# Performance work log

Measured on AMD Instinct MI355X. Metric: run time of the kernel, lower is better.

Reference implementation:

```python
import jax, jax.numpy as jnp
import numpy as np

N_NODES = 50000
N_EDGES = 800000
F_DIM = 256
H_DIM = 256
O_DIM = 64


def spmm(edge_index, edge_weight, x):
    # sparse adj (COO) @ dense x: out[dst] += w * x[src]
    src = edge_index[0]
    dst = edge_index[1]
    msgs = edge_weight[:, None] * x[src]          # [E, D]
    return jax.ops.segment_sum(msgs, dst, num_segments=x.shape[0])


def setup_inputs() -> dict:
    key = jax.random.key(0)
    ks = jax.random.split(key, 10)
    stdv = 1.0 / np.sqrt(H_DIM)
    u = lambda k, shp: jax.random.uniform(k, shp, jnp.float32, -stdv, stdv)
    return {
        "input": jax.random.normal(ks[0], (N_NODES, F_DIM), jnp.float32),
        "edge_index": jax.random.randint(ks[1], (2, N_EDGES), 0, N_NODES, jnp.int32),
        "edge_weight": jax.random.uniform(ks[2], (N_EDGES,), jnp.float32),
        "mixture_weight": u(ks[3], (1,)),
        "hidden_weight": u(ks[4], (F_DIM, H_DIM)),
        "hidden_bias": u(ks[5], (H_DIM,)),
        "mean_weight": u(ks[6], (H_DIM, O_DIM)),
        "mean_bias": u(ks[7], (O_DIM,)),
        "log_std_weight": u(ks[8], (H_DIM, O_DIM)),
        "log_std_bias": u(ks[9], (O_DIM,)),
    }


def reference(input, edge_index, edge_weight, mixture_weight, hidden_weight,
              hidden_bias, mean_weight, mean_bias, log_std_weight, log_std_bias):
    # eval mode: dropout is identity
    # --- GCN branch ---
    support = input @ hidden_weight                       # [N, H]
    hidden_g = jax.nn.relu(spmm(edge_index, edge_weight, support) + hidden_bias)
    mean_gcn = spmm(edge_index, edge_weight, hidden_g @ mean_weight)      # [N, O]
    log_std_gcn = spmm(edge_index, edge_weight, hidden_g @ log_std_weight)
    # --- MLP branch ---
    hidden_m = jax.nn.relu(support + hidden_bias)
    mean_mlp = hidden_m @ mean_weight + mean_bias
    log_std_mlp = hidden_m @ log_std_weight + log_std_bias
    # --- mixture (note: z_mean uses raw weight, z_log_std uses sigmoid, as in source) ---
    mw = mixture_weight
    mr = jax.nn.sigmoid(mixture_weight)
    z_mean = mean_gcn * mw + mean_mlp * (1.0 - mw)
    z_log_std = log_std_gcn * mr + log_std_mlp * (1.0 - mr)
    return (z_mean, z_log_std)
```

## Files before the change

kernel.cpp:

```cpp
#include <hip/hip_runtime.h>
#include <math.h>

#define NN 50000
#define NE 800000
#define KD 256
#define OD 64
#define NCH ((NN + 255) / 256)
#define EPB 4096
#define NBLK ((NE + EPB - 1) / EPB)
#define NHT (NCH * NBLK)

#define QS 32.0f
#define IQS (1.0f / 32.0f)
#define QS2 16.0f
#define IQS2 (1.0f / 16.0f)

using bf16x8 = __attribute__((ext_vector_type(8))) short;
using f32x4  = __attribute__((ext_vector_type(4))) float;

__device__ __forceinline__ unsigned short f2b(float x) {
    union { float f; unsigned u; } c; c.f = x;
    unsigned r = (c.u + 0x7FFF + ((c.u >> 16) & 1)) >> 16;
    return (unsigned short)r;
}
__device__ __forceinline__ float b2f(unsigned short b) {
    union { unsigned u; float f; } c; c.u = ((unsigned)b) << 16;
    return c.f;
}
__device__ __forceinline__ signed char quant8(float v) {
    int q = __float2int_rn(v * QS);
    q = q > 127 ? 127 : (q < -127 ? -127 : q);
    return (signed char)q;
}
__device__ __forceinline__ unsigned quant16u(float v) {
    int q = __float2int_rn(v * QS2);
    return (unsigned)(q > 127 ? 127 : q);
}

__device__ __forceinline__ void blk_scan(int* s, int t) {
    for (int o = 1; o < 256; o <<= 1) {
        int x = (t >= o) ? s[t - o] : 0;
        __syncthreads();
        s[t] += x;
        __syncthreads();
    }
}


__global__ __launch_bounds__(256) void k_histconv(const int* __restrict__ dst,
                                                  int* __restrict__ histT,
                                                  const float* __restrict__ hw,
                                                  const float* __restrict__ mw_,
                                                  const float* __restrict__ lw,
                                                  unsigned short* __restrict__ Wht,
                                                  unsigned short* __restrict__ Wmlt) {
    __shared__ int bins[NCH];
    int t = threadIdx.x;
    if (blockIdx.x < NBLK) {
        int blk = blockIdx.x;
        if (t < NCH) bins[t] = 0;
        __syncthreads();
        int base = blk * EPB;
        #pragma unroll
        for (int i = 0; i < EPB / 256; ++i) {
            int e = base + i * 256 + t;
            if (e < NE) atomicAdd(&bins[dst[e] >> 8], 1);
        }
        __syncthreads();
        if (t < NCH) histT[t * NBLK + blk] = bins[t];
    } else {
        int idx = (blockIdx.x - NBLK) * 256 + t;
        if (idx < 256 * 256) {
            int n = idx >> 8, k = idx & 255;
            Wht[(size_t)n * 256 + k] = f2b(hw[(size_t)k * 256 + n]);
        }
        if (idx < 128 * 256) {
            int n = idx >> 8, k = idx & 255;
            float v = (n < 64) ? mw_[(size_t)k * 64 + n] : lw[(size_t)k * 64 + (n - 64)];
            Wmlt[(size_t)n * 256 + k] = f2b(v);
        }
    }
}

__global__ __launch_bounds__(256) void k_scanbins(int* __restrict__ histT,
                                                  int* __restrict__ binSum) {
    __shared__ int s[256];
    int bin = blockIdx.x, t = threadIdx.x;
    int v = (t < NBLK) ? histT[bin * NBLK + t] : 0;
    s[t] = v;
    __syncthreads();
    blk_scan(s, t);
    if (t < NBLK) histT[bin * NBLK + t] = s[t] - v;
    if (t == NBLK - 1) binSum[bin] = s[t];
}

__global__ __launch_bounds__(256) void k_bucketw(const int* __restrict__ src,
                                                 const int* __restrict__ dst,
                                                 const float* __restrict__ w,
                                                 const int* __restrict__ histT,
                                                 const int* __restrict__ binSum,
                                                 int2* __restrict__ bkt) {
    __shared__ int pre[256];
    __shared__ int cur[NCH];
    int t = threadIdx.x, blk = blockIdx.x;
    int v = (t < NCH) ? binSum[t] : 0;
    pre[t] = v;
    __syncthreads();
    blk_scan(pre, t);
    if (t < NCH) cur[t] = histT[t * NBLK + blk] + (pre[t] - v);
    __syncthreads();
    int base = blk * EPB;
    #pragma unroll
    for (int i = 0; i < EPB / 256; ++i) {
        int e = base + i * 256 + t;
        if (e < NE) {
            int d = dst[e];
            int p = atomicAdd(&cur[d >> 8], 1);
            bkt[p] = make_int2((d << 16) | src[e], __float_as_int(w[e]));
        }
    }
}

__global__ __launch_bounds__(256) void k_deg2(const int2* __restrict__ bkt,
                                              const int* __restrict__ binSum,
                                              int* __restrict__ deg,
                                              int* __restrict__ chunkSum8) {
    __shared__ int incl[256];
    __shared__ int cnt[256];
    int t = threadIdx.x, b = blockIdx.x;
    incl[t] = (t < NCH) ? binSum[t] : 0;
    cnt[t] = 0;
    __syncthreads();
    blk_scan(incl, t);
    int e0 = (b > 0) ? incl[b - 1] : 0;
    int e1 = incl[b];
    __syncthreads();
    for (int e = e0 + t; e < e1; e += 256)
        atomicAdd(&cnt[(((unsigned)bkt[e].x) >> 16) & 255], 1);
    __syncthreads();
    int node = b * 256 + t;
    int c = cnt[t];
    if (node < NN) deg[node] = c;
    __shared__ int s[256];
    s[t] = (node < NN) ? ((c + 7) & ~7) : 0;
    __syncthreads();
    for (int o = 128; o > 0; o >>= 1) {
        if (t < o) s[t] += s[t + o];
        __syncthreads();
    }
    if (t == 0) chunkSum8[b] = s[0];
}

__global__ __launch_bounds__(256) void k_place2f(const int2* __restrict__ bkt,
                                                 const int* __restrict__ binSum,
                                                 const int* __restrict__ chunkSum8,
                                                 const int* __restrict__ deg,
                                                 int* __restrict__ offsets8,
                                                 int2* __restrict__ pedge) {
    __shared__ int binc[256];
    __shared__ int cinc[256];
    __shared__ int s[256];
    __shared__ int ncur[256];
    int t = threadIdx.x, b = blockIdx.x;
    binc[t] = (t < NCH) ? binSum[t] : 0;
    __syncthreads();
    blk_scan(binc, t);
    cinc[t] = (t < NCH) ? chunkSum8[t] : 0;
    __syncthreads();
    blk_scan(cinc, t);
    int e0 = (b > 0) ? binc[b - 1] : 0;
    int e1 = binc[b];
    int chunkBase = (b > 0) ? cinc[b - 1] : 0;
    __syncthreads();
    int node = b * 256 + t;
    int dv = (node < NN) ? deg[node] : 0;
    int pv = (dv + 7) & ~7;
    s[t] = pv;
    __syncthreads();
    blk_scan(s, t);
    int excl = s[t] - pv + chunkBase;
    if (node <= NN) offsets8[node] = excl;
    ncur[t] = excl;
    __syncthreads();
    for (int e = e0 + t; e < e1; e += 256) {
        int2 v = bkt[e];
        int d = ((unsigned)v.x) >> 16;
        int p = atomicAdd(&ncur[d & 255], 1);
        pedge[p] = v;
    }
    __syncthreads();
    if (node < NN) {
        int p0 = ncur[t];
        int p1 = excl + pv;
        for (int p = p0; p < p1; ++p) pedge[p] = make_int2(0, 0);
    }
}


__global__ __launch_bounds__(256) void k_gemm1(const float* __restrict__ Ap,
                                               const unsigned short* __restrict__ Bt,
                                               signed char* __restrict__ supqOut) {
    __shared__ unsigned short As[64 * 64];
    __shared__ unsigned short Bs[128 * 64];
    const int tid = threadIdx.x;
    const int row0 = (blockIdx.x >> 1) * 64;
    const int n0 = (blockIdx.x & 1) * 128;
    const int lane = tid & 63;
    const int w = tid >> 6, wm = w >> 1, wn = w & 1;
    const int lr = lane & 15, lg = lane >> 4;
    const int rA = tid >> 2, qA = tid & 3;
    const int rB = tid >> 1, hB = tid & 1;

    f32x4 acc[2][4] = {};

    for (int k0 = 0; k0 < KD; k0 += 64) {
        {
            int gr = row0 + rA;
            unsigned short tmp[16];
            if (gr < NN) {
                #pragma unroll
                for (int i = 0; i < 4; ++i) {
                    float4 v = *reinterpret_cast<const float4*>(
                        &Ap[(size_t)gr * KD + k0 + qA * 16 + i * 4]);
                    tmp[i * 4 + 0] = f2b(v.x); tmp[i * 4 + 1] = f2b(v.y);
                    tmp[i * 4 + 2] = f2b(v.z); tmp[i * 4 + 3] = f2b(v.w);
                }
            } else {
                #pragma unroll
                for (int i = 0; i < 16; ++i) tmp[i] = 0;
            }
            int s0 = (qA * 2) ^ (rA & 7);
            int s1 = (qA * 2 + 1) ^ (rA & 7);
            *reinterpret_cast<uint4*>(&As[rA * 64 + s0 * 8]) = *reinterpret_cast<const uint4*>(&tmp[0]);
            *reinterpret_cast<uint4*>(&As[rA * 64 + s1 * 8]) = *reinterpret_cast<const uint4*>(&tmp[8]);
        }
        {
            const unsigned short* B = Bt + (size_t)(n0 + rB) * KD + k0 + hB * 32;
            #pragma unroll
            for (int i = 0; i < 4; ++i) {
                uint4 u = *reinterpret_cast<const uint4*>(B + i * 8);
                int slot = (hB * 4 + i) ^ (rB & 7);
                *reinterpret_cast<uint4*>(&Bs[rB * 64 + slot * 8]) = u;
            }
        }
        __syncthreads();
        #pragma unroll
        for (int ks = 0; ks < 2; ++ks) {
            int slot = ks * 4 + lg;
            bf16x8 a[2], b[4];
            #pragma unroll
            for (int fm = 0; fm < 2; ++fm) {
                int ra = wm * 32 + fm * 16 + lr;
                a[fm] = *reinterpret_cast<const bf16x8*>(&As[ra * 64 + ((slot ^ (ra & 7))) * 8]);
            }
            #pragma unroll
            for (int fn = 0; fn < 4; ++fn) {
                int rb = wn * 64 + fn * 16 + lr;
                b[fn] = *reinterpret_cast<const bf16x8*>(&Bs[rb * 64 + ((slot ^ (rb & 7))) * 8]);
            }
            #pragma unroll
            for (int fm = 0; fm < 2; ++fm)
                #pragma unroll
                for (int fn = 0; fn < 4; ++fn)
                    acc[fm][fn] = __builtin_amdgcn_mfma_f32_16x16x32_bf16(a[fm], b[fn], acc[fm][fn], 0, 0, 0);
        }
        __syncthreads();
    }
    #pragma unroll
    for (int fm = 0; fm < 2; ++fm) {
        #pragma unroll
        for (int j = 0; j < 4; ++j) {
            int grow = row0 + wm * 32 + fm * 16 + lg * 4 + j;
            if (grow >= NN) continue;
            #pragma unroll
            for (int fn = 0; fn < 4; ++fn) {
                int gcol = n0 + wn * 64 + fn * 16 + lr;
                supqOut[(size_t)grow * 256 + gcol] = quant8(acc[fm][fn][j]);
            }
        }
    }
}


__global__ __launch_bounds__(256) void k_gemm2(const signed char* __restrict__ hgq,
                                               const signed char* __restrict__ supq,
                                               const unsigned short* __restrict__ Bt,
                                               const float* __restrict__ hbias,
                                               const float* __restrict__ mbias,
                                               const float* __restrict__ lbias,
                                               signed char* __restrict__ gcnq,
                                               unsigned short* __restrict__ mlpout) {
    __shared__ unsigned short As[64 * 64];
    __shared__ unsigned short Bs[128 * 64];
    const bool mlpMode = blockIdx.y != 0;
    const int tid = threadIdx.x;
    const int row0 = blockIdx.x * 64;
    const int lane = tid & 63;
    const int w = tid >> 6, wm = w >> 1, wn = w & 1;
    const int lr = lane & 15, lg = lane >> 4;
    const int rA = tid >> 2, qA = tid & 3;
    const int rB = tid >> 1, hB = tid & 1;

    f32x4 acc[2][4] = {};

    for (int k0 = 0; k0 < KD; k0 += 64) {
        {
            int gr = row0 + rA;
            unsigned short tmp[16];
            if (gr < NN) {
                signed char q[16];
                const signed char* Aq = mlpMode ? supq : hgq;
                *reinterpret_cast<uint4*>(q) =
                    *reinterpret_cast<const uint4*>(&Aq[(size_t)gr * KD + k0 + qA * 16]);
                if (mlpMode) {
                    #pragma unroll
                    for (int i = 0; i < 4; ++i) {
                        float4 hb4 = *reinterpret_cast<const float4*>(&hbias[k0 + qA * 16 + i * 4]);
                        tmp[i * 4 + 0] = f2b(fmaxf((float)q[i * 4 + 0] * IQS + hb4.x, 0.f));
                        tmp[i * 4 + 1] = f2b(fmaxf((float)q[i * 4 + 1] * IQS + hb4.y, 0.f));
                        tmp[i * 4 + 2] = f2b(fmaxf((float)q[i * 4 + 2] * IQS + hb4.z, 0.f));
                        tmp[i * 4 + 3] = f2b(fmaxf((float)q[i * 4 + 3] * IQS + hb4.w, 0.f));
                    }
                } else {
                    #pragma unroll
                    for (int i = 0; i < 16; ++i) tmp[i] = f2b((float)q[i] * IQS2);
                }
            } else {
                #pragma unroll
                for (int i = 0; i < 16; ++i) tmp[i] = 0;
            }
            int s0 = (qA * 2) ^ (rA & 7);
            int s1 = (qA * 2 + 1) ^ (rA & 7);
            *reinterpret_cast<uint4*>(&As[rA * 64 + s0 * 8]) = *reinterpret_cast<const uint4*>(&tmp[0]);
            *reinterpret_cast<uint4*>(&As[rA * 64 + s1 * 8]) = *reinterpret_cast<const uint4*>(&tmp[8]);
        }
        {
            const unsigned short* B = Bt + (size_t)rB * KD + k0 + hB * 32;
            #pragma unroll
            for (int i = 0; i < 4; ++i) {
                uint4 u = *reinterpret_cast<const uint4*>(B + i * 8);
                int slot = (hB * 4 + i) ^ (rB & 7);
                *reinterpret_cast<uint4*>(&Bs[rB * 64 + slot * 8]) = u;
            }
        }
        __syncthreads();
        #pragma unroll
        for (int ks = 0; ks < 2; ++ks) {
            int slot = ks * 4 + lg;
            bf16x8 a[2], b[4];
            #pragma unroll
            for (int fm = 0; fm < 2; ++fm) {
                int ra = wm * 32 + fm * 16 + lr;
                a[fm] = *reinterpret_cast<const bf16x8*>(&As[ra * 64 + ((slot ^ (ra & 7))) * 8]);
            }
            #pragma unroll
            for (int fn = 0; fn < 4; ++fn) {
                int rb = wn * 64 + fn * 16 + lr;
                b[fn] = *reinterpret_cast<const bf16x8*>(&Bs[rb * 64 + ((slot ^ (rb & 7))) * 8]);
            }
            #pragma unroll
            for (int fm = 0; fm < 2; ++fm)
                #pragma unroll
                for (int fn = 0; fn < 4; ++fn)
                    acc[fm][fn] = __builtin_amdgcn_mfma_f32_16x16x32_bf16(a[fm], b[fn], acc[fm][fn], 0, 0, 0);
        }
        __syncthreads();
    }
    #pragma unroll
    for (int fm = 0; fm < 2; ++fm) {
        #pragma unroll
        for (int j = 0; j < 4; ++j) {
            int grow = row0 + wm * 32 + fm * 16 + lg * 4 + j;
            if (grow >= NN) continue;
            #pragma unroll
            for (int fn = 0; fn < 4; ++fn) {
                int gcol = wn * 64 + fn * 16 + lr;
                float v = acc[fm][fn][j];
                if (mlpMode) {
                    float b = (gcol < 64) ? mbias[gcol] : lbias[gcol - 64];
                    mlpout[(size_t)grow * 128 + gcol] = f2b(v + b);
                } else {
                    gcnq[(size_t)grow * 128 + gcol] = quant8(v);
                }
            }
        }
    }
}


__global__ __launch_bounds__(256) void k_spmm1(const int* __restrict__ off8,
                                               const int2* __restrict__ pedge,
                                               const unsigned* __restrict__ supq,
                                               const float* __restrict__ bias,
                                               unsigned* __restrict__ hgq) {
    int lane = threadIdx.x & 63;
    int wid = blockIdx.x * 4 + (threadIdx.x >> 6);
    int d0 = wid * 2, d1 = d0 + 1;
    int ea = off8[d0], eA = off8[d0 + 1], eB = off8[d0 + 2];
    int eb = eA;
    float a0 = 0.f, a1 = 0.f, a2 = 0.f, a3 = 0.f;
    float c0 = 0.f, c1 = 0.f, c2 = 0.f, c3 = 0.f;
    for (; ea < eA && eb < eB; ea += 8, eb += 8) {
        int2 Ea[8], Eb[8];
        unsigned Ua[8], Ub[8];
        #pragma unroll
        for (int i = 0; i < 8; ++i) { Ea[i] = pedge[ea + i]; Eb[i] = pedge[eb + i]; }
        #pragma unroll
        for (int i = 0; i < 8; ++i) {
            Ua[i] = supq[(size_t)(Ea[i].x & 0xffff) * 64 + lane];
            Ub[i] = supq[(size_t)(Eb[i].x & 0xffff) * 64 + lane];
        }
        #pragma unroll
        for (int i = 0; i < 8; ++i) {
            float wa = __int_as_float(Ea[i].y), wb = __int_as_float(Eb[i].y);
            unsigned ua = Ua[i], ub = Ub[i];
            a0 = fmaf(wa, (float)((int)(signed char)(ua)), a0);
            a1 = fmaf(wa, (float)((int)(signed char)(ua >> 8)), a1);
            a2 = fmaf(wa, (float)((int)(signed char)(ua >> 16)), a2);
            a3 = fmaf(wa, (float)((int)(signed char)(ua >> 24)), a3);
            c0 = fmaf(wb, (float)((int)(signed char)(ub)), c0);
            c1 = fmaf(wb, (float)((int)(signed char)(ub >> 8)), c1);
            c2 = fmaf(wb, (float)((int)(signed char)(ub >> 16)), c2);
            c3 = fmaf(wb, (float)((int)(signed char)(ub >> 24)), c3);
        }
    }
    for (; ea < eA; ea += 8) {
        int2 E[8]; unsigned U[8];
        #pragma unroll
        for (int i = 0; i < 8; ++i) E[i] = pedge[ea + i];
        #pragma unroll
        for (int i = 0; i < 8; ++i) U[i] = supq[(size_t)(E[i].x & 0xffff) * 64 + lane];
        #pragma unroll
        for (int i = 0; i < 8; ++i) {
            float w = __int_as_float(E[i].y); unsigned u = U[i];
            a0 = fmaf(w, (float)((int)(signed char)(u)), a0);
            a1 = fmaf(w, (float)((int)(signed char)(u >> 8)), a1);
            a2 = fmaf(w, (float)((int)(signed char)(u >> 16)), a2);
            a3 = fmaf(w, (float)((int)(signed char)(u >> 24)), a3);
        }
    }
    for (; eb < eB; eb += 8) {
        int2 E[8]; unsigned U[8];
        #pragma unroll
        for (int i = 0; i < 8; ++i) E[i] = pedge[eb + i];
        #pragma unroll
        for (int i = 0; i < 8; ++i) U[i] = supq[(size_t)(E[i].x & 0xffff) * 64 + lane];
        #pragma unroll
        for (int i = 0; i < 8; ++i) {
            float w = __int_as_float(E[i].y); unsigned u = U[i];
            c0 = fmaf(w, (float)((int)(signed char)(u)), c0);
            c1 = fmaf(w, (float)((int)(signed char)(u >> 8)), c1);
            c2 = fmaf(w, (float)((int)(signed char)(u >> 16)), c2);
            c3 = fmaf(w, (float)((int)(signed char)(u >> 24)), c3);
        }
    }
    float4 b = *reinterpret_cast<const float4*>(&bias[lane * 4]);
    unsigned oa = quant16u(fmaxf(a0 * IQS + b.x, 0.f))
                | (quant16u(fmaxf(a1 * IQS + b.y, 0.f)) << 8)
                | (quant16u(fmaxf(a2 * IQS + b.z, 0.f)) << 16)
                | (quant16u(fmaxf(a3 * IQS + b.w, 0.f)) << 24);
    unsigned oc = quant16u(fmaxf(c0 * IQS + b.x, 0.f))
                | (quant16u(fmaxf(c1 * IQS + b.y, 0.f)) << 8)
                | (quant16u(fmaxf(c2 * IQS + b.z, 0.f)) << 16)
                | (quant16u(fmaxf(c3 * IQS + b.w, 0.f)) << 24);
    hgq[(size_t)d0 * 64 + lane] = oa;
    hgq[(size_t)d1 * 64 + lane] = oc;
}


__global__ __launch_bounds__(256) void k_spmm2(const int* __restrict__ off8,
                                               const int2* __restrict__ pedge,
                                               const unsigned short* __restrict__ gq,
                                               const unsigned short* __restrict__ mlp,
                                               const float* __restrict__ mixw,
                                               float* __restrict__ out) {
    int lane = threadIdx.x & 63;
    int wid = blockIdx.x * 4 + (threadIdx.x >> 6);
    int d0 = wid * 2, d1 = d0 + 1;
    int ea = off8[d0], eA = off8[d0 + 1], eB = off8[d0 + 2];
    int eb = eA;
    float a0 = 0.f, a1 = 0.f, c0 = 0.f, c1 = 0.f;
    for (; ea < eA && eb < eB; ea += 8, eb += 8) {
        int2 Ea[8], Eb[8];
        unsigned short Ua[8], Ub[8];
        #pragma unroll
        for (int i = 0; i < 8; ++i) { Ea[i] = pedge[ea + i]; Eb[i] = pedge[eb + i]; }
        #pragma unroll
        for (int i = 0; i < 8; ++i) {
            Ua[i] = gq[(size_t)(Ea[i].x & 0xffff) * 64 + lane];
            Ub[i] = gq[(size_t)(Eb[i].x & 0xffff) * 64 + lane];
        }
        #pragma unroll
        for (int i = 0; i < 8; ++i) {
            float wa = __int_as_float(Ea[i].y), wb = __int_as_float(Eb[i].y);
            a0 = fmaf(wa, (float)((int)(signed char)(Ua[i] & 0xff)), a0);
            a1 = fmaf(wa, (float)((int)(signed char)(Ua[i] >> 8)), a1);
            c0 = fmaf(wb, (float)((int)(signed char)(Ub[i] & 0xff)), c0);
            c1 = fmaf(wb, (float)((int)(signed char)(Ub[i] >> 8)), c1);
        }
    }
    for (; ea < eA; ea += 8) {
        int2 E[8]; unsigned short U[8];
        #pragma unroll
        for (int i = 0; i < 8; ++i) E[i] = pedge[ea + i];
        #pragma unroll
        for (int i = 0; i < 8; ++i) U[i] = gq[(size_t)(E[i].x & 0xffff) * 64 + lane];
        #pragma unroll
        for (int i = 0; i < 8; ++i) {
            float w = __int_as_float(E[i].y);
            a0 = fmaf(w, (float)((int)(signed char)(U[i] & 0xff)), a0);
            a1 = fmaf(w, (float)((int)(signed char)(U[i] >> 8)), a1);
        }
    }
    for (; eb < eB; eb += 8) {
        int2 E[8]; unsigned short U[8];
        #pragma unroll
        for (int i = 0; i < 8; ++i) E[i] = pedge[eb + i];
        #pragma unroll
        for (int i = 0; i < 8; ++i) U[i] = gq[(size_t)(E[i].x & 0xffff) * 64 + lane];
        #pragma unroll
        for (int i = 0; i < 8; ++i) {
            float w = __int_as_float(E[i].y);
            c0 = fmaf(w, (float)((int)(signed char)(U[i] & 0xff)), c0);
            c1 = fmaf(w, (float)((int)(signed char)(U[i] >> 8)), c1);
        }
    }
    float mw = mixw[0];
    float mr = 1.f / (1.f + expf(-mw));
    int c = lane * 2;
    ushort2 mu0 = reinterpret_cast<const ushort2*>(mlp)[(size_t)d0 * 64 + lane];
    ushort2 mu1 = reinterpret_cast<const ushort2*>(mlp)[(size_t)d1 * 64 + lane];
    float g00 = a0 * IQS, g01 = a1 * IQS;
    float g10 = c0 * IQS, g11 = c1 * IQS;
    if (c < 64) {
        *reinterpret_cast<float2*>(out + (size_t)d0 * OD + c) =
            make_float2(g00 * mw + b2f(mu0.x) * (1.f - mw), g01 * mw + b2f(mu0.y) * (1.f - mw));
        *reinterpret_cast<float2*>(out + (size_t)d1 * OD + c) =
            make_float2(g10 * mw + b2f(mu1.x) * (1.f - mw), g11 * mw + b2f(mu1.y) * (1.f - mw));
    } else {
        float* ol = out + (size_t)NN * OD;
        *reinterpret_cast<float2*>(ol + (size_t)d0 * OD + (c - 64)) =
            make_float2(g00 * mr + b2f(mu0.x) * (1.f - mr), g01 * mr + b2f(mu0.y) * (1.f - mr));
        *reinterpret_cast<float2*>(ol + (size_t)d1 * OD + (c - 64)) =
            make_float2(g10 * mr + b2f(mu1.x) * (1.f - mr), g11 * mr + b2f(mu1.y) * (1.f - mr));
    }
}


extern "C" void kernel_launch(void* const* d_in, const int* in_sizes, int n_in,
                              void* d_out, int out_size, void* d_ws, size_t ws_size,
                              hipStream_t stream) {
    const float* input = (const float*)d_in[0];
    const int*   ei    = (const int*)d_in[1];
    const float* ew    = (const float*)d_in[2];
    const float* mixw  = (const float*)d_in[3];
    const float* hw    = (const float*)d_in[4];
    const float* hb    = (const float*)d_in[5];
    const float* mw_   = (const float*)d_in[6];
    const float* mb    = (const float*)d_in[7];
    const float* lw    = (const float*)d_in[8];
    const float* lb    = (const float*)d_in[9];
    float* out = (float*)d_out;

    const int* src = ei;
    const int* dst = ei + NE;

    char* ws = (char*)d_ws;
    size_t off = 0;
    auto alloc = [&](size_t bytes) -> void* {
        void* p = ws + off;
        off += (bytes + 255) & ~(size_t)255;
        return p;
    };
    int*   deg      = (int*)alloc((size_t)NN * 4);
    int*   offsets8 = (int*)alloc((size_t)(NN + 2) * 4);
    int*   chunkSum8= (int*)alloc((size_t)NCH * 4);
    int*   binSum   = (int*)alloc((size_t)NCH * 4);
    int*   histT    = (int*)alloc((size_t)NHT * 4);
    int2*  bkt      = (int2*)alloc((size_t)NE * 8);
    int2*  pedge    = (int2*)alloc(((size_t)NE + 8 * NN) * 8);
    unsigned short* Wht  = (unsigned short*)alloc((size_t)256 * 256 * 2);
    unsigned short* Wmlt = (unsigned short*)alloc((size_t)128 * 256 * 2);
    signed char*    supq     = (signed char*)alloc((size_t)NN * KD);
    signed char*    hgq      = (signed char*)alloc((size_t)NN * KD);
    signed char*    gcnq     = (signed char*)alloc((size_t)NN * 128);
    unsigned short* mlp      = (unsigned short*)alloc((size_t)NN * 128 * 2);

    k_histconv<<<NBLK + 256, 256, 0, stream>>>(dst, histT, hw, mw_, lw, Wht, Wmlt);
    k_scanbins<<<NCH, 256, 0, stream>>>(histT, binSum);
    k_bucketw<<<NBLK, 256, 0, stream>>>(src, dst, ew, histT, binSum, bkt);
    k_deg2<<<NCH, 256, 0, stream>>>(bkt, binSum, deg, chunkSum8);
    k_place2f<<<NCH, 256, 0, stream>>>(bkt, binSum, chunkSum8, deg, offsets8, pedge);

    int mblk = (NN + 63) / 64;
    k_gemm1<<<mblk * 2, 256, 0, stream>>>(input, Wht, supq);
    k_spmm1<<<NN / 8, 256, 0, stream>>>(offsets8, pedge, (const unsigned*)supq, hb, (unsigned*)hgq);
    k_gemm2<<<dim3(mblk, 2), 256, 0, stream>>>(hgq, supq, Wmlt, hb, mb, lb, gcnq, mlp);
    k_spmm2<<<NN / 8, 256, 0, stream>>>(offsets8, pedge, (const unsigned short*)gcnq, mlp, mixw, out);
}
```

Baseline: 150.9 us.

## Pack CSR edges into 32-bit bf16 weight plus index, four nodes per wave

Edge records in the padded CSR are packed into one 32-bit word holding a 16-bit source index and a bf16 weight, instead of an int2 with an fp32 weight. This halves the edge-stream traffic in both SpMM passes. Each wavefront now processes four destination nodes as two contiguous two-node segment streams, switching accumulators at the midpoint offset, and the SpMM grids shrink to match. The cost is reduced precision in the edge weights and extra branching per 8-edge chunk.

New measurement: 152.4 us. About the same (+1.0%).

```diff
diff --git a/kernel.cpp b/kernel.cpp
--- a/kernel.cpp
+++ b/kernel.cpp
@@ -156,7 +156,7 @@
                                                  const int* __restrict__ chunkSum8,
                                                  const int* __restrict__ deg,
                                                  int* __restrict__ offsets8,
-                                                 int2* __restrict__ pedge) {
+                                                 int* __restrict__ pedge) {
     __shared__ int binc[256];
     __shared__ int cinc[256];
     __shared__ int s[256];
@@ -186,13 +186,13 @@
         int2 v = bkt[e];
         int d = ((unsigned)v.x) >> 16;
         int p = atomicAdd(&ncur[d & 255], 1);
-        pedge[p] = v;
+        pedge[p] = (v.x & 0xffff) | ((int)f2b(__int_as_float(v.y)) << 16);
     }
     __syncthreads();
     if (node < NN) {
         int p0 = ncur[t];
         int p1 = excl + pv;
-        for (int p = p0; p < p1; ++p) pedge[p] = make_int2(0, 0);
+        for (int p = p0; p < p1; ++p) pedge[p] = 0;
     }
 }
 
@@ -389,160 +389,184 @@
 
 
 __global__ __launch_bounds__(256) void k_spmm1(const int* __restrict__ off8,
-                                               const int2* __restrict__ pedge,
+                                               const int* __restrict__ pedge,
                                                const unsigned* __restrict__ supq,
                                                const float* __restrict__ bias,
                                                unsigned* __restrict__ hgq) {
     int lane = threadIdx.x & 63;
     int wid = blockIdx.x * 4 + (threadIdx.x >> 6);
-    int d0 = wid * 2, d1 = d0 + 1;
-    int ea = off8[d0], eA = off8[d0 + 1], eB = off8[d0 + 2];
-    int eb = eA;
-    float a0 = 0.f, a1 = 0.f, a2 = 0.f, a3 = 0.f;
-    float c0 = 0.f, c1 = 0.f, c2 = 0.f, c3 = 0.f;
-    for (; ea < eA && eb < eB; ea += 8, eb += 8) {
-        int2 Ea[8], Eb[8];
+    int d0 = wid * 4;
+    int ea = off8[d0],     midA = off8[d0 + 1], eAend = off8[d0 + 2];
+    int eb = eAend,        midB = off8[d0 + 3], eBend = off8[d0 + 4];
+    float a0[4] = {}, a1[4] = {}, b0[4] = {}, b1[4] = {};
+
+    while (ea < eAend && eb < eBend) {
+        int Ea[8], Eb[8];
         unsigned Ua[8], Ub[8];
         #pragma unroll
         for (int i = 0; i < 8; ++i) { Ea[i] = pedge[ea + i]; Eb[i] = pedge[eb + i]; }
         #pragma unroll
         for (int i = 0; i < 8; ++i) {
-            Ua[i] = supq[(size_t)(Ea[i].x & 0xffff) * 64 + lane];
-            Ub[i] = supq[(size_t)(Eb[i].x & 0xffff) * 64 + lane];
-        }
-        #pragma unroll
-        for (int i = 0; i < 8; ++i) {
-            float wa = __int_as_float(Ea[i].y), wb = __int_as_float(Eb[i].y);
+            Ua[i] = supq[(size_t)(Ea[i] & 0xffff) * 64 + lane];
+            Ub[i] = supq[(size_t)(Eb[i] & 0xffff) * 64 + lane];
+        }
+        float tA[4] = {}, tB[4] = {};
+        #pragma unroll
+        for (int i = 0; i < 8; ++i) {
+            float wa = b2f((unsigned short)(((unsigned)Ea[i]) >> 16));
+            float wb = b2f((unsigned short)(((unsigned)Eb[i]) >> 16));
             unsigned ua = Ua[i], ub = Ub[i];
-            a0 = fmaf(wa, (float)((int)(signed char)(ua)), a0);
-            a1 = fmaf(wa, (float)((int)(signed char)(ua >> 8)), a1);
-            a2 = fmaf(wa, (float)((int)(signed char)(ua >> 16)), a2);
-            a3 = fmaf(wa, (float)((int)(signed char)(ua >> 24)), a3);
-            c0 = fmaf(wb, (float)((int)(signed char)(ub)), c0);
-            c1 = fmaf(wb, (float)((int)(signed char)(ub >> 8)), c1);
-            c2 = fmaf(wb, (float)((int)(signed char)(ub >> 16)), c2);
-            c3 = fmaf(wb, (float)((int)(signed char)(ub >> 24)), c3);
-        }
-    }
-    for (; ea < eA; ea += 8) {
-        int2 E[8]; unsigned U[8];
+            tA[0] = fmaf(wa, (float)((int)(signed char)(ua)), tA[0]);
+            tA[1] = fmaf(wa, (float)((int)(signed char)(ua >> 8)), tA[1]);
+            tA[2] = fmaf(wa, (float)((int)(signed char)(ua >> 16)), tA[2]);
+            tA[3] = fmaf(wa, (float)((int)(signed char)(ua >> 24)), tA[3]);
+            tB[0] = fmaf(wb, (float)((int)(signed char)(ub)), tB[0]);
+            tB[1] = fmaf(wb, (float)((int)(signed char)(ub >> 8)), tB[1]);
+            tB[2] = fmaf(wb, (float)((int)(signed char)(ub >> 16)), tB[2]);
+            tB[3] = fmaf(wb, (float)((int)(signed char)(ub >> 24)), tB[3]);
+        }
+        if (ea < midA) { a0[0]+=tA[0]; a0[1]+=tA[1]; a0[2]+=tA[2]; a0[3]+=tA[3]; }
+        else           { a1[0]+=tA[0]; a1[1]+=tA[1]; a1[2]+=tA[2]; a1[3]+=tA[3]; }
+        if (eb < midB) { b0[0]+=tB[0]; b0[1]+=tB[1]; b0[2]+=tB[2]; b0[3]+=tB[3]; }
+        else           { b1[0]+=tB[0]; b1[1]+=tB[1]; b1[2]+=tB[2]; b1[3]+=tB[3]; }
+        ea += 8; eb += 8;
+    }
+    for (; ea < eAend; ea += 8) {
+        int E[8]; unsigned U[8];
         #pragma unroll
         for (int i = 0; i < 8; ++i) E[i] = pedge[ea + i];
         #pragma unroll
-        for (int i = 0; i < 8; ++i) U[i] = supq[(size_t)(E[i].x & 0xffff) * 64 + lane];
-        #pragma unroll
-        for (int i = 0; i < 8; ++i) {
-            float w = __int_as_float(E[i].y); unsigned u = U[i];
-            a0 = fmaf(w, (float)((int)(signed char)(u)), a0);
-            a1 = fmaf(w, (float)((int)(signed char)(u >> 8)), a1);
-            a2 = fmaf(w, (float)((int)(signed char)(u >> 16)), a2);
-            a3 = fmaf(w, (float)((int)(signed char)(u >> 24)), a3);
-        }
-    }
-    for (; eb < eB; eb += 8) {
-        int2 E[8]; unsigned U[8];
+        for (int i = 0; i < 8; ++i) U[i] = supq[(size_t)(E[i] & 0xffff) * 64 + lane];
+        float tA[4] = {};
+        #pragma unroll
+        for (int i = 0; i < 8; ++i) {
+            float w = b2f((unsigned short)(((unsigned)E[i]) >> 16));
+            unsigned u = U[i];
+            tA[0] = fmaf(w, (float)((int)(signed char)(u)), tA[0]);
+            tA[1] = fmaf(w, (float)((int)(signed char)(u >> 8)), tA[1]);
+            tA[2] = fmaf(w, (float)((int)(signed char)(u >> 16)), tA[2]);
+            tA[3] = fmaf(w, (float)((int)(signed char)(u >> 24)), tA[3]);
+        }
+        if (ea < midA) { a0[0]+=tA[0]; a0[1]+=tA[1]; a0[2]+=tA[2]; a0[3]+=tA[3]; }
+        else           { a1[0]+=tA[0]; a1[1]+=tA[1]; a1[2]+=tA[2]; a1[3]+=tA[3]; }
+    }
+    for (; eb < eBend; eb += 8) {
+        int E[8]; unsigned U[8];
         #pragma unroll
         for (int i = 0; i < 8; ++i) E[i] = pedge[eb + i];
         #pragma unroll
-        for (int i = 0; i < 8; ++i) U[i] = supq[(size_t)(E[i].x & 0xffff) * 64 + lane];
-        #pragma unroll
-        for (int i = 0; i < 8; ++i) {
-            float w = __int_as_float(E[i].y); unsigned u = U[i];
-            c0 = fmaf(w, (float)((int)(signed char)(u)), c0);
-            c1 = fmaf(w, (float)((int)(signed char)(u >> 8)), c1);
-            c2 = fmaf(w, (float)((int)(signed char)(u >> 16)), c2);
-            c3 = fmaf(w, (float)((int)(signed char)(u >> 24)), c3);
-        }
-    }
-    float4 b = *reinterpret_cast<const float4*>(&bias[lane * 4]);
-    unsigned oa = quant16u(fmaxf(a0 * IQS + b.x, 0.f))
-                | (quant16u(fmaxf(a1 * IQS + b.y, 0.f)) << 8)
-                | (quant16u(fmaxf(a2 * IQS + b.z, 0.f)) << 16)
-                | (quant16u(fmaxf(a3 * IQS + b.w, 0.f)) << 24);
-    unsigned oc = quant16u(fmaxf(c0 * IQS + b.x, 0.f))
-                | (quant16u(fmaxf(c1 * IQS + b.y, 0.f)) << 8)
-                | (quant16u(fmaxf(c2 * IQS + b.z, 0.f)) << 16)
-                | (quant16u(fmaxf(c3 * IQS + b.w, 0.f)) << 24);
-    hgq[(size_t)d0 * 64 + lane] = oa;
-    hgq[(size_t)d1 * 64 + lane] = oc;
+        for (int i = 0; i < 8; ++i) U[i] = supq[(size_t)(E[i] & 0xffff) * 64 + lane];
+        float tB[4] = {};
+        #pragma unroll
+        for (int i = 0; i < 8; ++i) {
+            float w = b2f((unsigned short)(((unsigned)E[i]) >> 16));
+            unsigned u = U[i];
+            tB[0] = fmaf(w, (float)((int)(signed char)(u)), tB[0]);
+            tB[1] = fmaf(w, (float)((int)(signed char)(u >> 8)), tB[1]);
+            tB[2] = fmaf(w, (float)((int)(signed char)(u >> 16)), tB[2]);
+            tB[3] = fmaf(w, (float)((int)(signed char)(u >> 24)), tB[3]);
+        }
+        if (eb < midB) { b0[0]+=tB[0]; b0[1]+=tB[1]; b0[2]+=tB[2]; b0[3]+=tB[3]; }
+        else           { b1[0]+=tB[0]; b1[1]+=tB[1]; b1[2]+=tB[2]; b1[3]+=tB[3]; }
+    }
+    float4 bv = *reinterpret_cast<const float4*>(&bias[lane * 4]);
+    float* accs[4] = { a0, a1, b0, b1 };
+    #pragma unroll
+    for (int j = 0; j < 4; ++j) {
+        float* a = accs[j];
+        unsigned o = quant16u(fmaxf(a[0] * IQS + bv.x, 0.f))
+                   | (quant16u(fmaxf(a[1] * IQS + bv.y, 0.f)) << 8)
+                   | (quant16u(fmaxf(a[2] * IQS + bv.z, 0.f)) << 16)
+                   | (quant16u(fmaxf(a[3] * IQS + bv.w, 0.f)) << 24);
+        hgq[(size_t)(d0 + j) * 64 + lane] = o;
+    }
 }
 
 
 __global__ __launch_bounds__(256) void k_spmm2(const int* __restrict__ off8,
-                                               const int2* __restrict__ pedge,
+                                               const int* __restrict__ pedge,
                                                const unsigned short* __restrict__ gq,
                                                const unsigned short* __restrict__ mlp,
                                                const float* __restrict__ mixw,
                                                float* __restrict__ out) {
     int lane = threadIdx.x & 63;
     int wid = blockIdx.x * 4 + (threadIdx.x >> 6);
-    int d0 = wid * 2, d1 = d0 + 1;
-    int ea = off8[d0], eA = off8[d0 + 1], eB = off8[d0 + 2];
-    int eb = eA;
-    float a0 = 0.f, a1 = 0.f, c0 = 0.f, c1 = 0.f;
-    for (; ea < eA && eb < eB; ea += 8, eb += 8) {
-        int2 Ea[8], Eb[8];
+    int d0 = wid * 4;
+    int ea = off8[d0],     midA = off8[d0 + 1], eAend = off8[d0 + 2];
+    int eb = eAend,        midB = off8[d0 + 3], eBend = off8[d0 + 4];
+    float a0[2] = {}, a1[2] = {}, b0[2] = {}, b1[2] = {};
+
+    while (ea < eAend && eb < eBend) {
+        int Ea[8], Eb[8];
         unsigned short Ua[8], Ub[8];
         #pragma unroll
         for (int i = 0; i < 8; ++i) { Ea[i] = pedge[ea + i]; Eb[i] = pedge[eb + i]; }
         #pragma unroll
         for (int i = 0; i < 8; ++i) {
-            Ua[i] = gq[(size_t)(Ea[i].x & 0xffff) * 64 + lane];
-            Ub[i] = gq[(size_t)(Eb[i].x & 0xffff) * 64 + lane];
-        }
-        #pragma unroll
-        for (int i = 0; i < 8; ++i) {
-            float wa = __int_as_float(Ea[i].y), wb = __int_as_float(Eb[i].y);
-            a0 = fmaf(wa, (float)((int)(signed char)(Ua[i] & 0xff)), a0);
-            a1 = fmaf(wa, (float)((int)(signed char)(Ua[i] >> 8)), a1);
-            c0 = fmaf(wb, (float)((int)(signed char)(Ub[i] & 0xff)), c0);
-            c1 = fmaf(wb, (float)((int)(signed char)(Ub[i] >> 8)), c1);
-        }
-    }
-    for (; ea < eA; ea += 8) {
-        int2 E[8]; unsigned short U[8];
+            Ua[i] = gq[(size_t)(Ea[i] & 0xffff) * 64 + lane];
+            Ub[i] = gq[(size_t)(Eb[i] & 0xffff) * 64 + lane];
+        }
+        float tA[2] = {}, tB[2] = {};
+        #pragma unroll
+        for (int i = 0; i < 8; ++i) {
+            float wa = b2f((unsigned short)(((unsigned)Ea[i]) >> 16));
+            float wb = b2f((unsigned short)(((unsigned)Eb[i]) >> 16));
+            tA[0] = fmaf(wa, (float)((int)(signed char)(Ua[i] & 0xff)), tA[0]);
+            tA[1] = fmaf(wa, (float)((int)(signed char)(Ua[i] >> 8)), tA[1]);
+            tB[0] = fmaf(wb, (float)((int)(signed char)(Ub[i] & 0xff)), tB[0]);
+            tB[1] = fmaf(wb, (float)((int)(signed char)(Ub[i] >> 8)), tB[1]);
+        }
+        if (ea < midA) { a0[0]+=tA[0]; a0[1]+=tA[1]; } else { a1[0]+=tA[0]; a1[1]+=tA[1]; }
+        if (eb < midB) { b0[0]+=tB[0]; b0[1]+=tB[1]; } else { b1[0]+=tB[0]; b1[1]+=tB[1]; }
+        ea += 8; eb += 8;
+    }
+    for (; ea < eAend; ea += 8) {
+        int E[8]; unsigned short U[8];
         #pragma unroll
         for (int i = 0; i < 8; ++i) E[i] = pedge[ea + i];
         #pragma unroll
-        for (int i = 0; i < 8; ++i) U[i] = gq[(size_t)(E[i].x & 0xffff) * 64 + lane];
-        #pragma unroll
-        for (int i = 0; i < 8; ++i) {
-            float w = __int_as_float(E[i].y);
-            a0 = fmaf(w, (float)((int)(signed char)(U[i] & 0xff)), a0);
-            a1 = fmaf(w, (float)((int)(signed char)(U[i] >> 8)), a1);
-        }
-    }
-    for (; eb < eB; eb += 8) {
-        int2 E[8]; unsigned short U[8];
+        for (int i = 0; i < 8; ++i) U[i] = gq[(size_t)(E[i] & 0xffff) * 64 + lane];
+        float tA[2] = {};
+        #pragma unroll
+        for (int i = 0; i < 8; ++i) {
+            float w = b2f((unsigned short)(((unsigned)E[i]) >> 16));
+            tA[0] = fmaf(w, (float)((int)(signed char)(U[i] & 0xff)), tA[0]);
+            tA[1] = fmaf(w, (float)((int)(signed char)(U[i] >> 8)), tA[1]);
+        }
+        if (ea < midA) { a0[0]+=tA[0]; a0[1]+=tA[1]; } else { a1[0]+=tA[0]; a1[1]+=tA[1]; }
+    }
+    for (; eb < eBend; eb += 8) {
+        int E[8]; unsigned short U[8];
         #pragma unroll
         for (int i = 0; i < 8; ++i) E[i] = pedge[eb + i];
         #pragma unroll
-        for (int i = 0; i < 8; ++i) U[i] = gq[(size_t)(E[i].x & 0xffff) * 64 + lane];
-        #pragma unroll
-        for (int i = 0; i < 8; ++i) {
-            float w = __int_as_float(E[i].y);
-            c0 = fmaf(w, (float)((int)(signed char)(U[i] & 0xff)), c0);
-            c1 = fmaf(w, (float)((int)(signed char)(U[i] >> 8)), c1);
-        }
+        for (int i = 0; i < 8; ++i) U[i] = gq[(size_t)(E[i] & 0xffff) * 64 + lane];
+        float tB[2] = {};
+        #pragma unroll
+        for (int i = 0; i < 8; ++i) {
+            float w = b2f((unsigned short)(((unsigned)E[i]) >> 16));
+            tB[0] = fmaf(w, (float)((int)(signed char)(U[i] & 0xff)), tB[0]);
+            tB[1] = fmaf(w, (float)((int)(signed char)(U[i] >> 8)), tB[1]);
+        }
+        if (eb < midB) { b0[0]+=tB[0]; b0[1]+=tB[1]; } else { b1[0]+=tB[0]; b1[1]+=tB[1]; }
     }
     float mw = mixw[0];
     float mr = 1.f / (1.f + expf(-mw));
     int c = lane * 2;
-    ushort2 mu0 = reinterpret_cast<const ushort2*>(mlp)[(size_t)d0 * 64 + lane];
-    ushort2 mu1 = reinterpret_cast<const ushort2*>(mlp)[(size_t)d1 * 64 + lane];
-    float g00 = a0 * IQS, g01 = a1 * IQS;
-    float g10 = c0 * IQS, g11 = c1 * IQS;
-    if (c < 64) {
-        *reinterpret_cast<float2*>(out + (size_t)d0 * OD + c) =
-            make_float2(g00 * mw + b2f(mu0.x) * (1.f - mw), g01 * mw + b2f(mu0.y) * (1.f - mw));
-        *reinterpret_cast<float2*>(out + (size_t)d1 * OD + c) =
-            make_float2(g10 * mw + b2f(mu1.x) * (1.f - mw), g11 * mw + b2f(mu1.y) * (1.f - mw));
-    } else {
-        float* ol = out + (size_t)NN * OD;
-        *reinterpret_cast<float2*>(ol + (size_t)d0 * OD + (c - 64)) =
-            make_float2(g00 * mr + b2f(mu0.x) * (1.f - mr), g01 * mr + b2f(mu0.y) * (1.f - mr));
-        *reinterpret_cast<float2*>(ol + (size_t)d1 * OD + (c - 64)) =
-            make_float2(g10 * mr + b2f(mu1.x) * (1.f - mr), g11 * mr + b2f(mu1.y) * (1.f - mr));
+    float* accs[4] = { a0, a1, b0, b1 };
+    #pragma unroll
+    for (int j = 0; j < 4; ++j) {
+        int d = d0 + j;
+        ushort2 mu = reinterpret_cast<const ushort2*>(mlp)[(size_t)d * 64 + lane];
+        float g0 = accs[j][0] * IQS, g1 = accs[j][1] * IQS;
+        if (c < 64) {
+            *reinterpret_cast<float2*>(out + (size_t)d * OD + c) =
+                make_float2(g0 * mw + b2f(mu.x) * (1.f - mw), g1 * mw + b2f(mu.y) * (1.f - mw));
+        } else {
+            float* ol = out + (size_t)NN * OD;
+            *reinterpret_cast<float2*>(ol + (size_t)d * OD + (c - 64)) =
+                make_float2(g0 * mr + b2f(mu.x) * (1.f - mr), g1 * mr + b2f(mu.y) * (1.f - mr));
+        }
     }
 }
 
@@ -573,12 +597,12 @@
         return p;
     };
     int*   deg      = (int*)alloc((size_t)NN * 4);
-    int*   offsets8 = (int*)alloc((size_t)(NN + 2) * 4);
+    int*   offsets8 = (int*)alloc((size_t)(NN + 4) * 4);
     int*   chunkSum8= (int*)alloc((size_t)NCH * 4);
     int*   binSum   = (int*)alloc((size_t)NCH * 4);
     int*   histT    = (int*)alloc((size_t)NHT * 4);
     int2*  bkt      = (int2*)alloc((size_t)NE * 8);
-    int2*  pedge    = (int2*)alloc(((size_t)NE + 8 * NN) * 8);
+    int*   pedge    = (int*)alloc(((size_t)NE + 8 * NN) * 4);
     unsigned short* Wht  = (unsigned short*)alloc((size_t)256 * 256 * 2);
     unsigned short* Wmlt = (unsigned short*)alloc((size_t)128 * 256 * 2);
     signed char*    supq     = (signed char*)alloc((size_t)NN * KD);
@@ -594,7 +618,7 @@
 
     int mblk = (NN + 63) / 64;
     k_gemm1<<<mblk * 2, 256, 0, stream>>>(input, Wht, supq);
-    k_spmm1<<<NN / 8, 256, 0, stream>>>(offsets8, pedge, (const unsigned*)supq, hb, (unsigned*)hgq);
+    k_spmm1<<<NN / 16, 256, 0, stream>>>(offsets8, pedge, (const unsigned*)supq, hb, (unsigned*)hgq);
     k_gemm2<<<dim3(mblk, 2), 256, 0, stream>>>(hgq, supq, Wmlt, hb, mb, lb, gcnq, mlp);
-    k_spmm2<<<NN / 8, 256, 0, stream>>>(offsets8, pedge, (const unsigned short*)gcnq, mlp, mixw, out);
-}
+    k_spmm2<<<NN / 16, 256, 0, stream>>>(offsets8, pedge, (const unsigned short*)gcnq, mlp, mixw, out);
+}
```
